# Kernel tuning notes

Measured on AMD Instinct MI355X. Metric: run time of the kernel, lower is better.

## Reference

```python
import jax, jax.numpy as jnp
import numpy as np

N_BINS = 15


def setup_inputs() -> dict:
    key = jax.random.key(0)
    k1, k2 = jax.random.split(key)
    N, C = 131072, 1000
    labels = jax.random.randint(k1, (N,), 0, C, dtype=jnp.int64)
    logits = jax.random.normal(k2, (N, C), dtype=jnp.float32)
    return {"labels": labels, "logits": logits}


def reference(labels, logits):
    # softmax then (confidence, prediction) = max over classes
    probs = jax.nn.softmax(logits, axis=-1)            # [N, C]
    confidences = jnp.max(probs, axis=1)               # [N]
    predictions = jnp.argmax(probs, axis=1)            # [N]
    accuracies = (predictions == labels).astype(jnp.float32)

    bounds = jnp.linspace(0.0, 1.0, N_BINS + 1)
    lowers, uppers = bounds[:-1], bounds[1:]
    # bins are (lower, upper], matching gt/le in the torch code
    in_bin = (confidences[None, :] > lowers[:, None]) & (
        confidences[None, :] <= uppers[:, None]
    )                                                   # [n_bins, N]
    mask = in_bin.astype(jnp.float32)
    counts = mask.sum(axis=1)                           # [n_bins]
    n = jnp.float32(confidences.shape[0])
    prop_in_bin = counts / n
    sum_conf = mask @ confidences                       # [n_bins]
    sum_acc = mask @ accuracies                         # [n_bins]
    safe = jnp.maximum(counts, 1.0)
    gap = jnp.abs(sum_conf / safe - sum_acc / safe)
    ece = jnp.sum(jnp.where(counts > 0, gap * prop_in_bin, 0.0))
    return (100.0 * ece).reshape(1)  # percent=True
```

## Files before the change

### kernel.cpp

```cpp
#include <hip/hip_runtime.h>
#include <math.h>

#define NBINS 15
#define NGRP  (NBINS * 3)

__device__ __forceinline__ float exp2_fast(float x) {
#if __has_builtin(__builtin_amdgcn_exp2f)
    return __builtin_amdgcn_exp2f(x);
#else
    return exp2f(x);
#endif
}

template<int NCHUNK_CT>
__global__ __launch_bounds__(256) void ece_phase1(
        const float* __restrict__ logits,
        const int*   __restrict__ labels,
        float*       __restrict__ ws,
        int N, int C, int NB) {
    __shared__ float s_cnt[NBINS];
    __shared__ float s_conf[NBINS];
    __shared__ float s_acc[NBINS];

    const int tid = threadIdx.x;
    if (tid < NBINS) { s_cnt[tid] = 0.0f; s_conf[tid] = 0.0f; s_acc[tid] = 0.0f; }
    __syncthreads();

    const int lane   = tid & 63;
    const int wib    = tid >> 6;
    const int wpb    = blockDim.x >> 6;
    const int waveId = blockIdx.x * wpb + wib;
    const int nWaves = gridDim.x * wpb;
    const int nchunk = NCHUNK_CT ? NCHUNK_CT : (C >> 2);
    const float L2E  = 1.4426950408889634f;

    int vl[4];
    #pragma unroll
    for (int j = 0; j < 4; ++j) {
        int v = nchunk - 64 * j;
        vl[j] = v < 0 ? 0 : (v > 64 ? 64 : v);
    }

    auto loadrow = [&](float4* v, int r, int& lab) {
        const float4* rp = (const float4*)(logits + (size_t)r * (size_t)C);
        #pragma unroll
        for (int j = 0; j < 4; ++j) {
            int q = lane + 64 * j;
            q = (q < nchunk) ? q : (nchunk - 1);
            v[j] = rp[q];
        }
        lab = labels[r];
    };

    auto compute = [&](const float4* v, int lab) {
        float m = fmaxf(fmaxf(v[0].x, v[0].y), fmaxf(v[0].z, v[0].w));
        #pragma unroll
        for (int j = 1; j < 4; ++j)
            m = fmaxf(m, fmaxf(fmaxf(v[j].x, v[j].y), fmaxf(v[j].z, v[j].w)));
        #pragma unroll
        for (int msk = 32; msk; msk >>= 1) m = fmaxf(m, __shfl_xor(m, msk, 64));

        const float c0 = -m * L2E;
        float s = 0.0f;
        #pragma unroll
        for (int j = 0; j < 4; ++j) {
            float sj = exp2_fast(fmaf(v[j].x, L2E, c0))
                     + exp2_fast(fmaf(v[j].y, L2E, c0))
                     + exp2_fast(fmaf(v[j].z, L2E, c0))
                     + exp2_fast(fmaf(v[j].w, L2E, c0));
            if (NCHUNK_CT ? (vl[j] < 64) : true)
                sj = (lane < vl[j]) ? sj : 0.0f;
            s += sj;
        }
        #pragma unroll
        for (int msk = 32; msk; msk >>= 1) s += __shfl_xor(s, msk, 64);

        bool pred = false;
        #pragma unroll
        for (int j = 0; j < 4; ++j) {
            const int e0 = (lane + 64 * j) << 2;
            const int d  = lab - e0;
            if ((unsigned)d < 4u) {
                float val = (d == 0) ? v[j].x : (d == 1) ? v[j].y
                          : (d == 2) ? v[j].z : v[j].w;
                pred = (val == m);
            }
        }
        const bool hit = (__ballot(pred) != 0ull);

        if (lane == 0) {
            const float conf = 1.0f / s;
            int b = NBINS - 1;
            #pragma unroll
            for (int i = 0; i < NBINS; ++i) {
                float ub = (float)((double)(i + 1) / (double)NBINS);
                if (conf <= ub) { b = i; break; }
            }
            atomicAdd(&s_cnt[b],  1.0f);
            atomicAdd(&s_conf[b], conf);
            atomicAdd(&s_acc[b],  hit ? 1.0f : 0.0f);
        }
    };

    float4 A[4], B[4], Cb[4];
    int labA = 0, labB = 0, labC = 0;

    int  ra = waveId, rb = ra + nWaves;
    bool hA = (ra < N), hB = (rb < N);
    if (hA) loadrow(A, ra, labA);
    if (hB) loadrow(B, rb, labB);

    while (hA) {
        const int  rc = rb + nWaves; const bool hC = (rc < N);
        if (hC) loadrow(Cb, rc, labC);
        compute(A, labA);
        if (!hB) break;

        const int  rd = rc + nWaves; const bool hD = (rd < N);
        if (hD) loadrow(A, rd, labA);
        compute(B, labB);
        if (!hC) break;

        const int  re = rd + nWaves; const bool hE = (re < N);
        if (hE) loadrow(B, re, labB);
        compute(Cb, labC);
        if (!hD) break;

        ra = rd; rb = re; hA = hD; hB = hE;
    }

    __syncthreads();
    if (tid < NGRP) {
        const int stat = tid / NBINS;
        const int bin  = tid % NBINS;
        const float v  = (stat == 0) ? s_cnt[bin]
                       : (stat == 1) ? s_conf[bin] : s_acc[bin];
        ws[(size_t)tid * (size_t)NB + (size_t)blockIdx.x] = v;
    }
}

__global__ __launch_bounds__(256) void ece_phase2(
        const float* __restrict__ ws, float* __restrict__ sums, int NB) {
    __shared__ float s_w[4];
    const int g    = blockIdx.x;
    const int tid  = threadIdx.x;
    const int lane = tid & 63;
    const int wib  = tid >> 6;

    const float* p = ws + (size_t)g * (size_t)NB;
    float s = 0.0f;
    for (int i = tid; i < NB; i += 256) s += p[i];
    #pragma unroll
    for (int msk = 32; msk; msk >>= 1) s += __shfl_xor(s, msk, 64);
    if (lane == 0) s_w[wib] = s;
    __syncthreads();
    if (tid == 0) sums[g] = s_w[0] + s_w[1] + s_w[2] + s_w[3];
}

__global__ void ece_phase3(const float* __restrict__ sums,
                           float* __restrict__ out, int N) {
    if (threadIdx.x == 0 && blockIdx.x == 0) {
        float ece = 0.0f;
        for (int i = 0; i < NBINS; ++i) {
            float cnt = sums[i];
            float sc  = sums[NBINS + i];
            float sa  = sums[2 * NBINS + i];
            float safe = fmaxf(cnt, 1.0f);
            float gap  = fabsf(sc / safe - sa / safe);
            if (cnt > 0.0f) ece += gap * (cnt / (float)N);
        }
        out[0] = 100.0f * ece;
    }
}

extern "C" void kernel_launch(void* const* d_in, const int* in_sizes, int n_in,
                              void* d_out, int out_size, void* d_ws, size_t ws_size,
                              hipStream_t stream) {
    const int*   labels = (const int*)d_in[0];
    const float* logits = (const float*)d_in[1];
    float*       out    = (float*)d_out;
    float*       ws     = (float*)d_ws;

    const int N = in_sizes[0];
    const int C = in_sizes[1] / in_sizes[0];

    int NB = 2048;
    while (NB > 64 && (size_t)(NGRP * NB + NGRP) * sizeof(float) > ws_size)
        NB >>= 1;
    float* sums = ws + (size_t)NGRP * (size_t)NB;

    if (C == 1000)
        ece_phase1<250><<<NB, 256, 0, stream>>>(logits, labels, ws, N, C, NB);
    else
        ece_phase1<0><<<NB, 256, 0, stream>>>(logits, labels, ws, N, C, NB);

    ece_phase2<<<NGRP, 256, 0, stream>>>(ws, sums, NB);
    ece_phase3<<<1, 64, 0, stream>>>(sums, out, N);
}
```

Before: 105.7 us.

## Fold final ECE reduction into phase2 via last-block counter and halve grid

Removes the third kernel launch by having the last-finishing phase2 block, detected with an atomic counter and threadfences, compute the final ECE. The counter is reset inside phase1. The phase1 grid drops from 2048 to 1024 blocks, so each wave handles more rows and there are fewer per-block partials to reduce. The trade is a little launch overhead saved against less parallelism in the memory-bound main kernel.

After: 111.0 us. 5.0% more time.

```diff
diff --git a/kernel.cpp b/kernel.cpp
--- a/kernel.cpp
+++ b/kernel.cpp
@@ -17,6 +17,7 @@
         const float* __restrict__ logits,
         const int*   __restrict__ labels,
         float*       __restrict__ ws,
+        unsigned*    __restrict__ counter,
         int N, int C, int NB) {
     __shared__ float s_cnt[NBINS];
     __shared__ float s_conf[NBINS];
@@ -24,6 +25,7 @@
 
     const int tid = threadIdx.x;
     if (tid < NBINS) { s_cnt[tid] = 0.0f; s_conf[tid] = 0.0f; s_acc[tid] = 0.0f; }
+    if (blockIdx.x == 0 && tid == 63) *counter = 0u;
     __syncthreads();
 
     const int lane   = tid & 63;
@@ -140,7 +142,8 @@
 }
 
 __global__ __launch_bounds__(256) void ece_phase2(
-        const float* __restrict__ ws, float* __restrict__ sums, int NB) {
+        const float* __restrict__ ws, float* sums, unsigned* counter,
+        float* out, int NB, int N) {
     __shared__ float s_w[4];
     const int g    = blockIdx.x;
     const int tid  = threadIdx.x;
@@ -154,22 +157,25 @@
     for (int msk = 32; msk; msk >>= 1) s += __shfl_xor(s, msk, 64);
     if (lane == 0) s_w[wib] = s;
     __syncthreads();
-    if (tid == 0) sums[g] = s_w[0] + s_w[1] + s_w[2] + s_w[3];
-}
-
-__global__ void ece_phase3(const float* __restrict__ sums,
-                           float* __restrict__ out, int N) {
-    if (threadIdx.x == 0 && blockIdx.x == 0) {
-        float ece = 0.0f;
-        for (int i = 0; i < NBINS; ++i) {
-            float cnt = sums[i];
-            float sc  = sums[NBINS + i];
-            float sa  = sums[2 * NBINS + i];
-            float safe = fmaxf(cnt, 1.0f);
-            float gap  = fabsf(sc / safe - sa / safe);
-            if (cnt > 0.0f) ece += gap * (cnt / (float)N);
-        }
-        out[0] = 100.0f * ece;
+
+    if (tid == 0) {
+        sums[g] = s_w[0] + s_w[1] + s_w[2] + s_w[3];
+        __threadfence();
+        const unsigned old = atomicAdd(counter, 1u);
+        if (old == gridDim.x - 1) {
+            __threadfence();
+            volatile float* vs = sums;
+            float ece = 0.0f;
+            for (int i = 0; i < NBINS; ++i) {
+                float cnt = vs[i];
+                float sc  = vs[NBINS + i];
+                float sa  = vs[2 * NBINS + i];
+                float safe = fmaxf(cnt, 1.0f);
+                float gap  = fabsf(sc / safe - sa / safe);
+                if (cnt > 0.0f) ece += gap * (cnt / (float)N);
+            }
+            out[0] = 100.0f * ece;
+        }
     }
 }
 
@@ -184,16 +190,16 @@
     const int N = in_sizes[0];
     const int C = in_sizes[1] / in_sizes[0];
 
-    int NB = 2048;
-    while (NB > 64 && (size_t)(NGRP * NB + NGRP) * sizeof(float) > ws_size)
+    int NB = 1024;
+    while (NB > 64 && (size_t)(NGRP * NB + NGRP + 1) * sizeof(float) > ws_size)
         NB >>= 1;
-    float* sums = ws + (size_t)NGRP * (size_t)NB;
+    float*    sums    = ws + (size_t)NGRP * (size_t)NB;
+    unsigned* counter = (unsigned*)(sums + NGRP);
 
     if (C == 1000)
-        ece_phase1<250><<<NB, 256, 0, stream>>>(logits, labels, ws, N, C, NB);
+        ece_phase1<250><<<NB, 256, 0, stream>>>(logits, labels, ws, counter, N, C, NB);
     else
-        ece_phase1<0><<<NB, 256, 0, stream>>>(logits, labels, ws, N, C, NB);
-
-    ece_phase2<<<NGRP, 256, 0, stream>>>(ws, sums, NB);
-    ece_phase3<<<1, 64, 0, stream>>>(sums, out, N);
-}
+        ece_phase1<0><<<NB, 256, 0, stream>>>(logits, labels, ws, counter, N, C, NB);
+
+    ece_phase2<<<NGRP, 256, 0, stream>>>(ws, sums, counter, out, NB, N);
+}
```
